# Kernel optimization log

Measured on AMD Instinct MI355X. Metric: run time of the kernel, lower is better.

## Reference

```python
import jax, jax.numpy as jnp
import numpy as np

THRESHOLD = 0.5
NEG_POS_RATIO = 3


def cxcycz_to_xyz(c):
    return jnp.concatenate([c[..., :3] - c[..., 3:] / 2, c[..., :3] + c[..., 3:] / 2], axis=-1)


def xyz_to_cxcycz(x):
    return jnp.concatenate([(x[..., :3] + x[..., 3:]) / 2, x[..., 3:] - x[..., :3]], axis=-1)


def cxcycz_to_gcxgcygcz(c, priors):
    # SSD offset encoding (variance 0.1 / 0.2), 3D version
    return jnp.concatenate([
        (c[..., :3] - priors[..., :3]) / (priors[..., 3:] / 10.0),
        jnp.log(c[..., 3:] / priors[..., 3:]) * 5.0,
    ], axis=-1)


def jaccard3d(a, b):
    # a: [n,6] xyz boxes, b: [m,6] xyz boxes -> [n,m] IoU
    lo = jnp.maximum(a[:, None, :3], b[None, :, :3])
    hi = jnp.minimum(a[:, None, 3:], b[None, :, 3:])
    inter = jnp.prod(jnp.clip(hi - lo, 0.0, None), axis=-1)
    va = jnp.prod(a[:, 3:] - a[:, :3], axis=-1)
    vb = jnp.prod(b[:, 3:] - b[:, :3], axis=-1)
    return inter / (va[:, None] + vb[None, :] - inter)


def setup_inputs() -> dict:
    key = jax.random.key(0)
    ks = jax.random.split(key, 6)
    B, P, n_obj, n_classes = 16, 131072, 16, 2
    predicted_locs = jax.random.normal(ks[0], (B, P, 6), jnp.float32)
    predicted_scores = jax.random.normal(ks[1], (B, P, n_classes), jnp.float32)
    ctr = jax.random.uniform(ks[2], (B, n_obj, 3), minval=0.2, maxval=0.8)
    sz = jax.random.uniform(ks[3], (B, n_obj, 3), minval=0.05, maxval=0.2)
    boxes = jnp.concatenate([ctr - sz / 2, ctr + sz / 2], axis=-1)
    labels = jnp.ones((B, n_obj), jnp.int32)  # single foreground class (lesion)
    pctr = jax.random.uniform(ks[4], (P, 3), minval=0.0, maxval=1.0)
    psz = jax.random.uniform(ks[5], (P, 3), minval=0.05, maxval=0.3)
    priors_cxcycz = jnp.concatenate([pctr, psz], axis=-1)
    return {
        'predicted_locs': predicted_locs,
        'predicted_scores': predicted_scores,
        'boxes': boxes,
        'labels': labels,
        'priors_cxcycz': priors_cxcycz,
    }


def reference(predicted_locs, predicted_scores, boxes, labels, priors_cxcycz):
    B, P, n_classes = predicted_scores.shape
    n_obj = boxes.shape[1]
    priors_xyz = cxcycz_to_xyz(priors_cxcycz)

    def match(boxes_i, labels_i):
        ov = jaccard3d(boxes_i, priors_xyz)              # [n_obj, P]
        overlap_fp = ov.max(axis=0)                      # best overlap per prior
        object_fp = jnp.argmax(ov, axis=0)               # best object per prior
        prior_fo = jnp.argmax(ov, axis=1)                # best prior per object
        # force each object's best prior to be matched to that object
        object_fp = object_fp.at[prior_fo].set(jnp.arange(n_obj))
        overlap_fp = overlap_fp.at[prior_fo].set(1.0)
        lab = jnp.where(overlap_fp < THRESHOLD, 0, labels_i[object_fp])
        tl = cxcycz_to_gcxgcygcz(xyz_to_cxcycz(boxes_i[object_fp]), priors_cxcycz)
        return lab, tl

    true_classes, true_locs = jax.vmap(match)(boxes, labels)  # [B,P], [B,P,6]

    pos = true_classes > 0                               # [B,P]
    n_pos = pos.sum(axis=1)                              # [B]
    total_pos = n_pos.sum()

    # L1Loss(mean) over positive rows of [*,6]
    loc_abs = jnp.abs(predicted_locs - true_locs).sum(axis=-1)   # [B,P]
    loc_loss = (loc_abs * pos).sum() / (total_pos * 6).astype(predicted_locs.dtype)

    # per-prior cross-entropy
    logp = jax.nn.log_softmax(predicted_scores, axis=-1)
    conf_all = -jnp.take_along_axis(logp, true_classes[..., None], axis=-1)[..., 0]
    conf_all = jnp.where(true_classes < 0, 0.0, conf_all)  # ignored priors (soft mode only)
    conf_pos_sum = (conf_all * pos).sum()

    # hard-negative mining: zero out positives, sort each row descending, take top 3*n_pos
    conf_neg = jnp.where(pos, 0.0, conf_all)
    conf_neg_sorted = -jnp.sort(-conf_neg, axis=1)
    hard = jnp.arange(P)[None, :] < (NEG_POS_RATIO * n_pos)[:, None]
    conf_loss = (jnp.where(hard, conf_neg_sorted, 0.0).sum() + conf_pos_sum) / total_pos.astype(predicted_scores.dtype)
    return conf_loss, loc_loss
```

## Files before the change

kernel.cpp:

```cpp
#include <hip/hip_runtime.h>
#include <math.h>

#define MITEMS 2
#define LB 32


template <int NOBJ, bool FULL>
__global__ __launch_bounds__(256) void mbl_match(
    const float* __restrict__ boxes, const float* __restrict__ priors,
    unsigned long long* __restrict__ part_fo, unsigned char* __restrict__ best_u8,
    int P, int n_obj) {
  const int b = blockIdx.y;
  const int tid = threadIdx.x;
  __shared__ float4 s_box[NOBJ][2];
  __shared__ unsigned s_iou[8][257];
  __shared__ unsigned s_inv[8][257];
  __shared__ unsigned long long s_red2[8][33];

  for (int i = tid; i < NOBJ; i += 256) {
    float4 v0, v1;
    if (i < n_obj) {
      const float* bx = boxes + ((size_t)b * n_obj + i) * 6;
      const float l0 = bx[0], l1 = bx[1], l2 = bx[2];
      const float h0 = bx[3], h1 = bx[4], h2 = bx[5];
      v0 = make_float4(l0, l1, l2, h0);
      v1 = make_float4(h1, h2, ((h0 - l0) * (h1 - l1)) * (h2 - l2), 0.f);
    } else {
      v0 = make_float4(3e18f, 3e18f, 3e18f, 1e18f);
      v1 = make_float4(1e18f, 1e18f, 0.f, 0.f);
    }
    s_box[i][0] = v0;
    s_box[i][1] = v1;
  }
  __syncthreads();

  float lo0[MITEMS], lo1[MITEMS], lo2[MITEMS], hi0[MITEMS], hi1[MITEMS],
      hi2[MITEMS], vb[MITEMS];
  unsigned invp[MITEMS];
  const int base = blockIdx.x * (256 * MITEMS);
#pragma unroll
  for (int k = 0; k < MITEMS; ++k) {
    const int p = base + k * 256 + tid;
    if (FULL || p < P) {
      const float2 q0 = *(const float2*)(priors + (size_t)p * 6);
      const float2 q1 = *(const float2*)(priors + (size_t)p * 6 + 2);
      const float2 q2 = *(const float2*)(priors + (size_t)p * 6 + 4);
      lo0[k] = q0.x - q1.y * 0.5f; hi0[k] = q0.x + q1.y * 0.5f;
      lo1[k] = q0.y - q2.x * 0.5f; hi1[k] = q0.y + q2.x * 0.5f;
      lo2[k] = q1.x - q2.y * 0.5f; hi2[k] = q1.x + q2.y * 0.5f;
      vb[k] = (q1.y * q2.x) * q2.y;
      invp[k] = 0xFFFFFFFFu - (unsigned)p;
    } else {
      lo0[k] = lo1[k] = lo2[k] = 3e18f;
      hi0[k] = hi1[k] = hi2[k] = 3e18f;
      vb[k] = 0.f;
      invp[k] = 0u;
    }
  }

  float piou[NOBJ];
  unsigned pinv[NOBJ];
#pragma unroll
  for (int o = 0; o < NOBJ; ++o) { piou[o] = -1.0f; pinv[o] = 0u; }
  float bv[MITEMS];
  int bo[MITEMS];
#pragma unroll
  for (int k = 0; k < MITEMS; ++k) { bv[k] = -1.0f; bo[k] = 0; }

#pragma unroll
  for (int o = 0; o < NOBJ; ++o) {
    const float4 c0 = s_box[o][0];
    const float4 c1 = s_box[o][1];
#pragma unroll
    for (int k = 0; k < MITEMS; ++k) {
      const float d0 = fminf(c0.w, hi0[k]) - fmaxf(c0.x, lo0[k]);
      const float d1 = fminf(c1.x, hi1[k]) - fmaxf(c0.y, lo1[k]);
      const float d2 = fminf(c1.y, hi2[k]) - fmaxf(c0.z, lo2[k]);
      const float inter = (fmaxf(d0, 0.f) * fmaxf(d1, 0.f)) * fmaxf(d2, 0.f);
      const float un = (c1.z + vb[k]) - inter;
      const float iou = inter * __builtin_amdgcn_rcpf(un);
      if (iou > bv[k]) { bv[k] = iou; bo[k] = o; }
      if (iou > piou[o]) { piou[o] = iou; pinv[o] = invp[k]; }
    }
  }

#pragma unroll
  for (int k = 0; k < MITEMS; ++k) {
    const int p = base + k * 256 + tid;
    if (FULL || p < P)
      best_u8[(size_t)b * P + p] =
          (unsigned char)((unsigned)bo[k] | (bv[k] >= 0.5f ? 0x80u : 0u));
  }

  for (int pass = 0; pass < NOBJ / 8; ++pass) {
    if (pass > 0) __syncthreads();
#pragma unroll
    for (int o = 0; o < NOBJ; ++o) {
      if ((o >> 3) == pass) {
        s_iou[o & 7][tid] = __float_as_uint(piou[o]);
        s_inv[o & 7][tid] = pinv[o];
      }
    }
    __syncthreads();
    const int obj8 = tid >> 5, seg = tid & 31;
    unsigned long long m = 0ULL;
#pragma unroll
    for (int i = 0; i < 8; ++i) {
      const int idx = seg + 32 * i;
      const unsigned long long x =
          ((unsigned long long)s_iou[obj8][idx] << 32) | s_inv[obj8][idx];
      if (x > m) m = x;
    }
    s_red2[obj8][seg] = m;
    __syncthreads();
    if (tid < 8) {
      unsigned long long m2 = 0ULL;
      for (int i = 0; i < 32; ++i) {
        const unsigned long long x = s_red2[tid][i];
        if (x > m2) m2 = x;
      }
      const int o = pass * 8 + tid;
      if (o < n_obj)
        part_fo[((size_t)b * gridDim.x + blockIdx.x) * NOBJ + o] = m2;
    }
  }
}

__global__ __launch_bounds__(256) void mbl_reduce_fo(
    const unsigned long long* __restrict__ part_fo,
    unsigned char* __restrict__ best_u8,
    unsigned long long* __restrict__ zero_buf, int zero_words,
    int nblk, int n_obj, int nobjT, int P) {
  const int b = blockIdx.x;
  const int tid = threadIdx.x;
  {
    const int total = (int)gridDim.x * 256;
    for (int i = b * 256 + tid; i < zero_words; i += total) zero_buf[i] = 0ULL;
  }
  __shared__ unsigned s_win[64];
  const int j = tid & 15;
  for (int o0 = 0; o0 < n_obj; o0 += 16) {
    const int o = o0 + (tid >> 4);
    unsigned long long v = 0ULL;
    if (o < n_obj) {
      const unsigned long long* src = part_fo + (size_t)b * nblk * nobjT + o;
      for (int i = j; i < nblk; i += 16) {
        const unsigned long long x = src[(size_t)i * nobjT];
        if (x > v) v = x;
      }
    }
#pragma unroll
    for (int off = 1; off < 16; off <<= 1) {
      const unsigned long long w = __shfl_xor(v, off, 64);
      if (w > v) v = w;
    }
    if (j == 0 && o < n_obj)
      s_win[o] = 0xFFFFFFFFu - (unsigned)(v & 0xFFFFFFFFull);
  }
  __syncthreads();
  if (tid == 0) {
    for (int o = 0; o < n_obj; ++o)
      best_u8[(size_t)b * P + s_win[o]] = (unsigned char)(0x80u | (unsigned)o);
  }
}

template <int CC>
__global__ __launch_bounds__(256) void mbl_loss(
    const float* __restrict__ locs, const float* __restrict__ scores,
    const float* __restrict__ boxes, const int* __restrict__ labels,
    const float* __restrict__ priors, const unsigned char* __restrict__ best_u8,
    float* __restrict__ conf_neg, unsigned* __restrict__ hist0,
    int* __restrict__ n_pos, double* __restrict__ pconf, double* __restrict__ ploc,
    int P, int n_obj, int C) {
  const int b = blockIdx.y;
  const int tid = threadIdx.x;
  __shared__ float s_box[64][6];
  __shared__ int s_lab[64];
  __shared__ unsigned s_hist[4096];
  for (int i = tid; i < 4096; i += 256) s_hist[i] = 0u;
  for (int i = tid; i < n_obj * 6; i += 256)
    s_box[i / 6][i % 6] = boxes[(size_t)b * n_obj * 6 + i];
  for (int i = tid; i < n_obj; i += 256) s_lab[i] = labels[(size_t)b * n_obj + i];
  __syncthreads();

  const int chunk = (P + gridDim.x - 1) / gridDim.x;
  const int start = blockIdx.x * chunk;
  const int end = min(start + chunk, P);
  int np_l = 0;
  double cf_l = 0.0, lc_l = 0.0;
  for (int p = start + tid; p < end; p += 256) {
    const unsigned char bp = best_u8[(size_t)b * P + p];
    const int obj = bp & 0x7F;
    const int posf = bp >> 7;
    const int lab = posf ? s_lab[obj] : 0;

    float conf;
    if (CC == 2) {
      const float2 sc = *(const float2*)(scores + ((size_t)b * P + p) * 2);
      const float m = fmaxf(sc.x, sc.y);
      conf = (lab < 0) ? 0.f
                       : (m + __logf(__expf(sc.x - m) + __expf(sc.y - m)) -
                          ((lab == 0) ? sc.x : sc.y));
    } else {
      const float* sp = scores + ((size_t)b * P + p) * C;
      float m = sp[0];
      for (int c = 1; c < C; ++c) m = fmaxf(m, sp[c]);
      float se = 0.f;
      for (int c = 0; c < C; ++c) se += __expf(sp[c] - m);
      conf = (lab < 0) ? 0.f : (m + __logf(se) - sp[lab]);
    }

    float cn = conf;
    if (lab > 0) {
      np_l++;
      cf_l += (double)conf;
      const float* pr = priors + (size_t)p * 6;
      const float* pl = locs + ((size_t)b * P + p) * 6;
      float ls = 0.f;
      for (int i = 0; i < 3; ++i) {
        const float c0 = (s_box[obj][i] + s_box[obj][i + 3]) * 0.5f;
        const float szb = s_box[obj][i + 3] - s_box[obj][i];
        const float g = (c0 - pr[i]) / (pr[i + 3] / 10.0f);
        const float g2 = logf(szb / pr[i + 3]) * 5.0f;
        ls += fabsf(pl[i] - g) + fabsf(pl[i + 3] - g2);
      }
      lc_l += (double)ls;
      cn = 0.f;
    }
    conf_neg[(size_t)b * P + p] = cn;
    atomicAdd(&s_hist[__float_as_uint(cn) >> 20], 1u);
  }

  __shared__ int r_np[256];
  __shared__ double r_c[256];
  __shared__ double r_l[256];
  r_np[tid] = np_l;
  r_c[tid] = cf_l;
  r_l[tid] = lc_l;
  __syncthreads();
  for (int s = 128; s > 0; s >>= 1) {
    if (tid < s) {
      r_np[tid] += r_np[tid + s];
      r_c[tid] += r_c[tid + s];
      r_l[tid] += r_l[tid + s];
    }
    __syncthreads();
  }
  if (tid == 0 && r_np[0] > 0) {
    atomicAdd(&n_pos[b], r_np[0]);
    atomicAdd(&pconf[b], r_c[0]);
    atomicAdd(&ploc[b], r_l[0]);
  }
  for (int i = tid; i < 4096; i += 256)
    if (s_hist[i]) atomicAdd(&hist0[(size_t)b * 4096 + i], s_hist[i]);
}

template <int BINS>
__device__ void block_select(const unsigned* __restrict__ h, int remk,
                             unsigned* s_scan, int* s_out, unsigned* sel,
                             int* remk_o) {
  constexpr int BPT = BINS / 256;
  const int t = threadIdx.x;
  if (t == 0) { s_out[0] = BINS - 1; s_out[1] = 0; }
  unsigned mb[BPT];
  unsigned s = 0;
#pragma unroll
  for (int i = 0; i < BPT; ++i) { mb[i] = h[t * BPT + i]; s += mb[i]; }
  unsigned incl = s;
  s_scan[t] = incl;
  __syncthreads();
  for (int off = 1; off < 256; off <<= 1) {
    const unsigned add = (t >= off) ? s_scan[t - off] : 0u;
    __syncthreads();
    incl += add;
    s_scan[t] = incl;
    __syncthreads();
  }
  const unsigned total = s_scan[255];
  const unsigned R = total - incl;
  if (remk > 0 && R < (unsigned)remk && R + s >= (unsigned)remk) {
    unsigned acc = R;
    int sel_i = t * BPT, rk = 0;
    bool done = false;
#pragma unroll
    for (int i = BPT - 1; i >= 0; --i) {
      if (!done && acc + mb[i] >= (unsigned)remk) {
        sel_i = t * BPT + i;
        rk = remk - (int)acc;
        done = true;
      }
      if (!done) acc += mb[i];
    }
    s_out[0] = sel_i;
    s_out[1] = rk;
  }
  __syncthreads();
  *sel = (unsigned)s_out[0];
  *remk_o = s_out[1];
  __syncthreads();
}

__global__ __launch_bounds__(256) void mbl_hist1(
    const float* __restrict__ conf_neg, const int* __restrict__ n_pos,
    const unsigned* __restrict__ hist0, unsigned* __restrict__ hist1, int P) {
  const int b = blockIdx.y;
  const int tid = threadIdx.x;
  __shared__ unsigned s_scan[256];
  __shared__ int s_out[2];
  __shared__ unsigned s_hist[4096];
  int K = 3 * n_pos[b];
  if (K > P) K = P;
  unsigned sel0;
  int rem0;
  block_select<4096>(hist0 + (size_t)b * 4096, K, s_scan, s_out, &sel0, &rem0);
  for (int i = tid; i < 4096; i += 256) s_hist[i] = 0u;
  __syncthreads();
  const float* row = conf_neg + (size_t)b * P;
  const int n4 = P >> 2;
  const int per = (n4 + (int)gridDim.x - 1) / (int)gridDim.x;
  const int s4 = blockIdx.x * per, e4 = min(s4 + per, n4);
  for (int i = s4 + tid; i < e4; i += 256) {
    const float4 v = ((const float4*)row)[i];
    unsigned u;
    u = __float_as_uint(v.x); if ((u >> 20) == sel0) atomicAdd(&s_hist[(u >> 8) & 4095u], 1u);
    u = __float_as_uint(v.y); if ((u >> 20) == sel0) atomicAdd(&s_hist[(u >> 8) & 4095u], 1u);
    u = __float_as_uint(v.z); if ((u >> 20) == sel0) atomicAdd(&s_hist[(u >> 8) & 4095u], 1u);
    u = __float_as_uint(v.w); if ((u >> 20) == sel0) atomicAdd(&s_hist[(u >> 8) & 4095u], 1u);
  }
  if (blockIdx.x == 0)
    for (int p = (n4 << 2) + tid; p < P; p += 256) {
      const unsigned u = __float_as_uint(row[p]);
      if ((u >> 20) == sel0) atomicAdd(&s_hist[(u >> 8) & 4095u], 1u);
    }
  __syncthreads();
  for (int i = tid; i < 4096; i += 256)
    if (s_hist[i]) atomicAdd(&hist1[(size_t)b * 4096 + i], s_hist[i]);
}

__global__ __launch_bounds__(256) void mbl_sum(
    const float* __restrict__ conf_neg, const int* __restrict__ n_pos,
    const unsigned* __restrict__ hist0, const unsigned* __restrict__ hist1,
    const double* __restrict__ pconf, const double* __restrict__ ploc,
    double* __restrict__ phard, unsigned* __restrict__ counter,
    int P, int B, float* __restrict__ out) {
  const int b = blockIdx.y;
  const int tid = threadIdx.x;
  __shared__ unsigned s_scan[256];
  __shared__ int s_out[2];
  int K = 3 * n_pos[b];
  if (K > P) K = P;
  unsigned sel0, sel1;
  int rem0, rem1;
  block_select<4096>(hist0 + (size_t)b * 4096, K, s_scan, s_out, &sel0, &rem0);
  block_select<4096>(hist1 + (size_t)b * 4096, rem0, s_scan, s_out, &sel1, &rem1);
  const unsigned pref24 = (sel0 << 12) | sel1;
  const unsigned tb = (pref24 << 8) | 0xFFu;
  const float* row = conf_neg + (size_t)b * P;
  const int n4 = P >> 2;
  const int per = (n4 + (int)gridDim.x - 1) / (int)gridDim.x;
  const int s4 = blockIdx.x * per, e4 = min(s4 + per, n4);
  double local = 0.0;
  for (int i = s4 + tid; i < e4; i += 256) {
    const float4 v = ((const float4*)row)[i];
    if (__float_as_uint(v.x) > tb) local += (double)v.x;
    if (__float_as_uint(v.y) > tb) local += (double)v.y;
    if (__float_as_uint(v.z) > tb) local += (double)v.z;
    if (__float_as_uint(v.w) > tb) local += (double)v.w;
  }
  if (blockIdx.x == 0) {
    for (int p = (n4 << 2) + tid; p < P; p += 256) {
      const float v = row[p];
      if (__float_as_uint(v) > tb) local += (double)v;
    }
    if (tid == 0 && rem1 > 0)
      local += (double)rem1 * (double)__uint_as_float((pref24 << 8) | 0x80u);
  }
  __shared__ double red[256];
  red[tid] = local;
  __syncthreads();
  for (int s = 128; s > 0; s >>= 1) {
    if (tid < s) red[tid] += red[tid + s];
    __syncthreads();
  }
  if (tid == 0) {
    if (red[0] != 0.0) atomicAdd(&phard[b], red[0]);
    __threadfence();
    const unsigned done = atomicAdd(counter, 1u);
    if (done == gridDim.x * gridDim.y - 1) {
      double tp = 0.0, cs = 0.0, ls = 0.0, hs = 0.0;
      for (int i = 0; i < B; ++i) {
        tp += (double)n_pos[i];
        cs += pconf[i];
        ls += ploc[i];
        hs += atomicAdd(&phard[i], 0.0);
      }
      out[0] = (float)((hs + cs) / tp);
      out[1] = (float)(ls / (tp * 6.0));
    }
  }
}

extern "C" void kernel_launch(void* const* d_in, const int* in_sizes, int n_in,
                              void* d_out, int out_size, void* d_ws, size_t ws_size,
                              hipStream_t stream) {
  const float* locs = (const float*)d_in[0];
  const float* scores = (const float*)d_in[1];
  const float* boxes = (const float*)d_in[2];
  const int* labels = (const int*)d_in[3];
  const float* priors = (const float*)d_in[4];

  const long long sz_locs = (long long)in_sizes[0];
  const long long sz_scores = (long long)in_sizes[1];
  const long long sz_priors = (long long)in_sizes[4];
  const int P = (int)(sz_priors / 6);
  const int B = (int)(sz_locs / sz_priors);
  const int n_obj = in_sizes[3] / B;
  const int C = (int)(sz_scores * 6 / sz_locs);

  const int tile = 256 * MITEMS;
  const int nblk = (P + tile - 1) / tile;
  const int nobjT = (n_obj <= 16) ? 16 : ((n_obj <= 32) ? 32 : 64);

  char* ws = (char*)d_ws;
  size_t off = 0;
  double* pconf = (double*)(ws + off); off += (size_t)B * 8;
  double* ploc = (double*)(ws + off); off += (size_t)B * 8;
  double* phard = (double*)(ws + off); off += (size_t)B * 8;
  int* n_pos = (int*)(ws + off); off += ((size_t)B * 4 + 15) & ~(size_t)15;
  unsigned* counter = (unsigned*)(ws + off); off += 16;
  unsigned* hist0 = (unsigned*)(ws + off); off += (size_t)B * 4096 * 4;
  unsigned* hist1 = (unsigned*)(ws + off); off += (size_t)B * 4096 * 4;
  const size_t zero_bytes = off;
  float* conf_neg = (float*)(ws + off); off += ((size_t)B * P * 4 + 15) & ~(size_t)15;
  unsigned char* best_u8 = (unsigned char*)(ws + off);
  off += ((size_t)B * P + 15) & ~(size_t)15;
  unsigned long long* part_fo = (unsigned long long*)(ws + off);
  off += (size_t)B * nblk * nobjT * 8;
  (void)ws_size;

  const dim3 mgrid(nblk, B);
  const bool full = (P % tile) == 0;
  if (n_obj <= 16) {
    if (full) mbl_match<16, true><<<mgrid, 256, 0, stream>>>(boxes, priors, part_fo, best_u8, P, n_obj);
    else      mbl_match<16, false><<<mgrid, 256, 0, stream>>>(boxes, priors, part_fo, best_u8, P, n_obj);
  } else if (n_obj <= 32) {
    if (full) mbl_match<32, true><<<mgrid, 256, 0, stream>>>(boxes, priors, part_fo, best_u8, P, n_obj);
    else      mbl_match<32, false><<<mgrid, 256, 0, stream>>>(boxes, priors, part_fo, best_u8, P, n_obj);
  } else {
    if (full) mbl_match<64, true><<<mgrid, 256, 0, stream>>>(boxes, priors, part_fo, best_u8, P, n_obj);
    else      mbl_match<64, false><<<mgrid, 256, 0, stream>>>(boxes, priors, part_fo, best_u8, P, n_obj);
  }

  mbl_reduce_fo<<<B, 256, 0, stream>>>(part_fo, best_u8, (unsigned long long*)d_ws,
                                       (int)(zero_bytes / 8), nblk, n_obj, nobjT, P);

  const dim3 lgrid(LB, B);
  if (C == 2)
    mbl_loss<2><<<lgrid, 256, 0, stream>>>(locs, scores, boxes, labels, priors,
                                           best_u8, conf_neg, hist0, n_pos, pconf, ploc,
                                           P, n_obj, C);
  else
    mbl_loss<0><<<lgrid, 256, 0, stream>>>(locs, scores, boxes, labels, priors,
                                           best_u8, conf_neg, hist0, n_pos, pconf, ploc,
                                           P, n_obj, C);

  mbl_hist1<<<lgrid, 256, 0, stream>>>(conf_neg, n_pos, hist0, hist1, P);
  mbl_sum<<<lgrid, 256, 0, stream>>>(conf_neg, n_pos, hist0, hist1, pconf, ploc,
                                     phard, counter, P, B, (float*)d_out);
}
```

Baseline: 88.60 us.

## Track max IoU only in match, recover argmax prior in a second pass

The match kernel now keeps only a 32-bit max IoU per object instead of a packed 64-bit (iou, index) pair, and reduces it with shuffles and a global atomicMax. A new recover kernel recomputes IoU only in blocks whose partial max equals the global max, using bit-exact rounding intrinsics, and atomically selects the lowest winning prior index. The loss kernel then applies the forced-positive override by comparing each prior against the per-object winner list, replacing the serial scatter in the old reduce kernel. This lightens register pressure and inner-loop work in match, at the cost of an extra kernel launch, a memset, and a per-prior 16-way compare in the loss kernel.

```diff
diff --git a/kernel.cpp b/kernel.cpp
--- a/kernel.cpp
+++ b/kernel.cpp
@@ -2,66 +2,86 @@
 #include <math.h>
 
 #define MITEMS 2
+#define TILE 512
 #define LB 32
 
+
+__device__ __forceinline__ void prep_prior(const float* __restrict__ pr,
+                                           float& lo0, float& lo1, float& lo2,
+                                           float& hi0, float& hi1, float& hi2,
+                                           float& vb) {
+  const float2 q0 = *(const float2*)(pr);
+  const float2 q1 = *(const float2*)(pr + 2);
+  const float2 q2 = *(const float2*)(pr + 4);
+  const float h0 = __fmul_rn(q1.y, 0.5f);
+  const float h1 = __fmul_rn(q2.x, 0.5f);
+  const float h2 = __fmul_rn(q2.y, 0.5f);
+  lo0 = __fadd_rn(q0.x, -h0); hi0 = __fadd_rn(q0.x, h0);
+  lo1 = __fadd_rn(q0.y, -h1); hi1 = __fadd_rn(q0.y, h1);
+  lo2 = __fadd_rn(q1.x, -h2); hi2 = __fadd_rn(q1.x, h2);
+  vb = __fmul_rn(__fmul_rn(q1.y, q2.x), q2.y);
+}
+
+__device__ __forceinline__ void make_box(const float* __restrict__ bx,
+                                         float4& c0, float4& c1) {
+  const float l0 = bx[0], l1 = bx[1], l2 = bx[2];
+  const float h0 = bx[3], h1 = bx[4], h2 = bx[5];
+  c0 = make_float4(l0, l1, l2, h0);
+  const float vol = __fmul_rn(
+      __fmul_rn(__fadd_rn(h0, -l0), __fadd_rn(h1, -l1)), __fadd_rn(h2, -l2));
+  c1 = make_float4(h1, h2, vol, 0.f);
+}
+
+__device__ __forceinline__ float iou6(float lo0, float lo1, float lo2, float hi0,
+                                      float hi1, float hi2, float vb,
+                                      const float4& c0, const float4& c1) {
+  const float d0 = __fadd_rn(fminf(c0.w, hi0), -fmaxf(c0.x, lo0));
+  const float d1 = __fadd_rn(fminf(c1.x, hi1), -fmaxf(c0.y, lo1));
+  const float d2 = __fadd_rn(fminf(c1.y, hi2), -fmaxf(c0.z, lo2));
+  const float e0 = fmaxf(d0, 0.f), e1 = fmaxf(d1, 0.f), e2 = fmaxf(d2, 0.f);
+  const float inter = __fmul_rn(__fmul_rn(e0, e1), e2);
+  const float un = __fadd_rn(__fadd_rn(c1.z, vb), -inter);
+  return __fmul_rn(inter, __builtin_amdgcn_rcpf(un));
+}
 
 template <int NOBJ, bool FULL>
 __global__ __launch_bounds__(256) void mbl_match(
     const float* __restrict__ boxes, const float* __restrict__ priors,
-    unsigned long long* __restrict__ part_fo, unsigned char* __restrict__ best_u8,
-    int P, int n_obj) {
+    unsigned* __restrict__ part_max, unsigned* __restrict__ M,
+    unsigned char* __restrict__ best_u8, int P, int n_obj) {
   const int b = blockIdx.y;
   const int tid = threadIdx.x;
   __shared__ float4 s_box[NOBJ][2];
-  __shared__ unsigned s_iou[8][257];
-  __shared__ unsigned s_inv[8][257];
-  __shared__ unsigned long long s_red2[8][33];
-
+  __shared__ unsigned s_tr[16][264];
   for (int i = tid; i < NOBJ; i += 256) {
-    float4 v0, v1;
     if (i < n_obj) {
-      const float* bx = boxes + ((size_t)b * n_obj + i) * 6;
-      const float l0 = bx[0], l1 = bx[1], l2 = bx[2];
-      const float h0 = bx[3], h1 = bx[4], h2 = bx[5];
-      v0 = make_float4(l0, l1, l2, h0);
-      v1 = make_float4(h1, h2, ((h0 - l0) * (h1 - l1)) * (h2 - l2), 0.f);
+      make_box(boxes + ((size_t)b * n_obj + i) * 6, s_box[i][0], s_box[i][1]);
     } else {
-      v0 = make_float4(3e18f, 3e18f, 3e18f, 1e18f);
-      v1 = make_float4(1e18f, 1e18f, 0.f, 0.f);
-    }
-    s_box[i][0] = v0;
-    s_box[i][1] = v1;
+      s_box[i][0] = make_float4(3e18f, 3e18f, 3e18f, 1e18f);
+      s_box[i][1] = make_float4(1e18f, 1e18f, 1.0f, 0.f);
+    }
   }
   __syncthreads();
 
   float lo0[MITEMS], lo1[MITEMS], lo2[MITEMS], hi0[MITEMS], hi1[MITEMS],
       hi2[MITEMS], vb[MITEMS];
-  unsigned invp[MITEMS];
-  const int base = blockIdx.x * (256 * MITEMS);
+  const int base = blockIdx.x * TILE;
 #pragma unroll
   for (int k = 0; k < MITEMS; ++k) {
     const int p = base + k * 256 + tid;
     if (FULL || p < P) {
-      const float2 q0 = *(const float2*)(priors + (size_t)p * 6);
-      const float2 q1 = *(const float2*)(priors + (size_t)p * 6 + 2);
-      const float2 q2 = *(const float2*)(priors + (size_t)p * 6 + 4);
-      lo0[k] = q0.x - q1.y * 0.5f; hi0[k] = q0.x + q1.y * 0.5f;
-      lo1[k] = q0.y - q2.x * 0.5f; hi1[k] = q0.y + q2.x * 0.5f;
-      lo2[k] = q1.x - q2.y * 0.5f; hi2[k] = q1.x + q2.y * 0.5f;
-      vb[k] = (q1.y * q2.x) * q2.y;
-      invp[k] = 0xFFFFFFFFu - (unsigned)p;
+      prep_prior(priors + (size_t)p * 6, lo0[k], lo1[k], lo2[k], hi0[k], hi1[k],
+                 hi2[k], vb[k]);
     } else {
       lo0[k] = lo1[k] = lo2[k] = 3e18f;
       hi0[k] = hi1[k] = hi2[k] = 3e18f;
       vb[k] = 0.f;
-      invp[k] = 0u;
     }
   }
 
   float piou[NOBJ];
-  unsigned pinv[NOBJ];
-#pragma unroll
-  for (int o = 0; o < NOBJ; ++o) { piou[o] = -1.0f; pinv[o] = 0u; }
+#pragma unroll
+  for (int o = 0; o < NOBJ; ++o) piou[o] = 0.f;
   float bv[MITEMS];
   int bo[MITEMS];
 #pragma unroll
@@ -73,14 +93,12 @@
     const float4 c1 = s_box[o][1];
 #pragma unroll
     for (int k = 0; k < MITEMS; ++k) {
-      const float d0 = fminf(c0.w, hi0[k]) - fmaxf(c0.x, lo0[k]);
-      const float d1 = fminf(c1.x, hi1[k]) - fmaxf(c0.y, lo1[k]);
-      const float d2 = fminf(c1.y, hi2[k]) - fmaxf(c0.z, lo2[k]);
-      const float inter = (fmaxf(d0, 0.f) * fmaxf(d1, 0.f)) * fmaxf(d2, 0.f);
-      const float un = (c1.z + vb[k]) - inter;
-      const float iou = inter * __builtin_amdgcn_rcpf(un);
-      if (iou > bv[k]) { bv[k] = iou; bo[k] = o; }
-      if (iou > piou[o]) { piou[o] = iou; pinv[o] = invp[k]; }
+      const float iou = iou6(lo0[k], lo1[k], lo2[k], hi0[k], hi1[k], hi2[k],
+                             vb[k], c0, c1);
+      const bool g = iou > bv[k];
+      bv[k] = g ? iou : bv[k];
+      bo[k] = g ? o : bo[k];
+      piou[o] = fmaxf(piou[o], iou);
     }
   }
 
@@ -92,75 +110,74 @@
           (unsigned char)((unsigned)bo[k] | (bv[k] >= 0.5f ? 0x80u : 0u));
   }
 
-  for (int pass = 0; pass < NOBJ / 8; ++pass) {
-    if (pass > 0) __syncthreads();
-#pragma unroll
-    for (int o = 0; o < NOBJ; ++o) {
-      if ((o >> 3) == pass) {
-        s_iou[o & 7][tid] = __float_as_uint(piou[o]);
-        s_inv[o & 7][tid] = pinv[o];
+  for (int o0 = 0; o0 < NOBJ; o0 += 16) {
+    if (o0) __syncthreads();
+#pragma unroll
+    for (int o = 0; o < NOBJ; ++o)
+      if (o >= o0 && o < o0 + 16) s_tr[o - o0][tid] = __float_as_uint(piou[o]);
+    __syncthreads();
+    const int obj = tid >> 4, j = tid & 15;
+    unsigned m = 0u;
+#pragma unroll
+    for (int i = 0; i < 16; ++i) m = max(m, s_tr[obj][j + 16 * i]);
+#pragma unroll
+    for (int off = 1; off < 16; off <<= 1) m = max(m, __shfl_xor(m, off, 64));
+    if (j == 0) {
+      const int o = o0 + obj;
+      if (o < n_obj) {
+        part_max[((size_t)b * gridDim.x + blockIdx.x) * NOBJ + o] = m;
+        atomicMax(&M[(size_t)b * 64 + o], m);
       }
     }
-    __syncthreads();
-    const int obj8 = tid >> 5, seg = tid & 31;
-    unsigned long long m = 0ULL;
-#pragma unroll
-    for (int i = 0; i < 8; ++i) {
-      const int idx = seg + 32 * i;
-      const unsigned long long x =
-          ((unsigned long long)s_iou[obj8][idx] << 32) | s_inv[obj8][idx];
-      if (x > m) m = x;
-    }
-    s_red2[obj8][seg] = m;
-    __syncthreads();
-    if (tid < 8) {
-      unsigned long long m2 = 0ULL;
-      for (int i = 0; i < 32; ++i) {
-        const unsigned long long x = s_red2[tid][i];
-        if (x > m2) m2 = x;
-      }
-      const int o = pass * 8 + tid;
-      if (o < n_obj)
-        part_fo[((size_t)b * gridDim.x + blockIdx.x) * NOBJ + o] = m2;
-    }
-  }
-}
-
-__global__ __launch_bounds__(256) void mbl_reduce_fo(
-    const unsigned long long* __restrict__ part_fo,
-    unsigned char* __restrict__ best_u8,
-    unsigned long long* __restrict__ zero_buf, int zero_words,
-    int nblk, int n_obj, int nobjT, int P) {
-  const int b = blockIdx.x;
+  }
+}
+
+template <bool FULL>
+__global__ __launch_bounds__(256) void mbl_recover(
+    const float* __restrict__ boxes, const float* __restrict__ priors,
+    const unsigned* __restrict__ part_max, const unsigned* __restrict__ M,
+    unsigned* __restrict__ win, unsigned long long* __restrict__ zero_buf,
+    int zero_words, int P, int n_obj, int nobjT) {
+  const int b = blockIdx.y;
+  const int blk = blockIdx.x;
   const int tid = threadIdx.x;
   {
-    const int total = (int)gridDim.x * 256;
-    for (int i = b * 256 + tid; i < zero_words; i += total) zero_buf[i] = 0ULL;
-  }
-  __shared__ unsigned s_win[64];
-  const int j = tid & 15;
-  for (int o0 = 0; o0 < n_obj; o0 += 16) {
-    const int o = o0 + (tid >> 4);
-    unsigned long long v = 0ULL;
-    if (o < n_obj) {
-      const unsigned long long* src = part_fo + (size_t)b * nblk * nobjT + o;
-      for (int i = j; i < nblk; i += 16) {
-        const unsigned long long x = src[(size_t)i * nobjT];
-        if (x > v) v = x;
+    const int gid = b * gridDim.x + blk;
+    const int total = (int)(gridDim.x * gridDim.y) * 256;
+    for (int i = gid * 256 + tid; i < zero_words; i += total) zero_buf[i] = 0ULL;
+  }
+  __shared__ unsigned s_mu[64];
+  __shared__ int s_hit[64];
+  if (tid < 64) {
+    unsigned mu = 0u;
+    int hit = 0;
+    if (tid < n_obj && tid < nobjT) {
+      mu = M[(size_t)b * 64 + tid];
+      const unsigned pm = part_max[((size_t)b * gridDim.x + blk) * nobjT + tid];
+      hit = (pm == mu);
+    }
+    s_mu[tid] = mu;
+    s_hit[tid] = hit;
+  }
+  __syncthreads();
+
+  const int base = blk * TILE;
+  for (int o = 0; o < n_obj; ++o) {
+    if (!s_hit[o]) continue;
+    float4 c0, c1;
+    make_box(boxes + ((size_t)b * n_obj + o) * 6, c0, c1);
+    const unsigned target = s_mu[o];
+#pragma unroll
+    for (int k = 0; k < MITEMS; ++k) {
+      const int p = base + k * 256 + tid;
+      if (FULL || p < P) {
+        float lo0, lo1, lo2, hi0, hi1, hi2, vb;
+        prep_prior(priors + (size_t)p * 6, lo0, lo1, lo2, hi0, hi1, hi2, vb);
+        const float iou = iou6(lo0, lo1, lo2, hi0, hi1, hi2, vb, c0, c1);
+        if (__float_as_uint(iou) == target)
+          atomicMax(&win[(size_t)b * 64 + o], 0xFFFFFFFFu - (unsigned)p);
       }
     }
-#pragma unroll
-    for (int off = 1; off < 16; off <<= 1) {
-      const unsigned long long w = __shfl_xor(v, off, 64);
-      if (w > v) v = w;
-    }
-    if (j == 0 && o < n_obj)
-      s_win[o] = 0xFFFFFFFFu - (unsigned)(v & 0xFFFFFFFFull);
-  }
-  __syncthreads();
-  if (tid == 0) {
-    for (int o = 0; o < n_obj; ++o)
-      best_u8[(size_t)b * P + s_win[o]] = (unsigned char)(0x80u | (unsigned)o);
   }
 }
 
@@ -168,20 +185,32 @@
 __global__ __launch_bounds__(256) void mbl_loss(
     const float* __restrict__ locs, const float* __restrict__ scores,
     const float* __restrict__ boxes, const int* __restrict__ labels,
-    const float* __restrict__ priors, const unsigned char* __restrict__ best_u8,
-    float* __restrict__ conf_neg, unsigned* __restrict__ hist0,
-    int* __restrict__ n_pos, double* __restrict__ pconf, double* __restrict__ ploc,
-    int P, int n_obj, int C) {
+    const float* __restrict__ priors, const unsigned* __restrict__ win,
+    const unsigned char* __restrict__ best_u8, float* __restrict__ conf_neg,
+    unsigned* __restrict__ hist0, int* __restrict__ n_pos,
+    double* __restrict__ pconf, double* __restrict__ ploc, int P, int n_obj,
+    int C) {
   const int b = blockIdx.y;
   const int tid = threadIdx.x;
   __shared__ float s_box[64][6];
   __shared__ int s_lab[64];
+  __shared__ unsigned s_fo[64];
   __shared__ unsigned s_hist[4096];
   for (int i = tid; i < 4096; i += 256) s_hist[i] = 0u;
   for (int i = tid; i < n_obj * 6; i += 256)
     s_box[i / 6][i % 6] = boxes[(size_t)b * n_obj * 6 + i];
-  for (int i = tid; i < n_obj; i += 256) s_lab[i] = labels[(size_t)b * n_obj + i];
-  __syncthreads();
+  for (int i = tid; i < n_obj; i += 256) {
+    s_lab[i] = labels[(size_t)b * n_obj + i];
+    s_fo[i] = 0xFFFFFFFFu - win[(size_t)b * 64 + i];
+  }
+  __syncthreads();
+
+  unsigned fo_r[16];
+  const bool small_obj = (n_obj <= 16);
+  if (small_obj) {
+#pragma unroll
+    for (int o = 0; o < 16; ++o) fo_r[o] = (o < n_obj) ? s_fo[o] : 0xFFFFFFFEu;
+  }
 
   const int chunk = (P + gridDim.x - 1) / gridDim.x;
   const int start = blockIdx.x * chunk;
@@ -190,8 +219,16 @@
   double cf_l = 0.0, lc_l = 0.0;
   for (int p = start + tid; p < end; p += 256) {
     const unsigned char bp = best_u8[(size_t)b * P + p];
-    const int obj = bp & 0x7F;
-    const int posf = bp >> 7;
+    int obj = bp & 0x7F;
+    int posf = bp >> 7;
+    if (small_obj) {
+#pragma unroll
+      for (int o = 0; o < 16; ++o)
+        if (fo_r[o] == (unsigned)p) { obj = o; posf = 1; }
+    } else {
+      for (int o = 0; o < n_obj; ++o)
+        if (s_fo[o] == (unsigned)p) { obj = o; posf = 1; }
+    }
     const int lab = posf ? s_lab[obj] : 0;
 
     float conf;
@@ -341,8 +378,8 @@
     const float* __restrict__ conf_neg, const int* __restrict__ n_pos,
     const unsigned* __restrict__ hist0, const unsigned* __restrict__ hist1,
     const double* __restrict__ pconf, const double* __restrict__ ploc,
-    double* __restrict__ phard, unsigned* __restrict__ counter,
-    int P, int B, float* __restrict__ out) {
+    double* __restrict__ phard, unsigned* __restrict__ counter, int P, int B,
+    float* __restrict__ out) {
   const int b = blockIdx.y;
   const int tid = threadIdx.x;
   __shared__ unsigned s_scan[256];
@@ -417,8 +454,7 @@
   const int n_obj = in_sizes[3] / B;
   const int C = (int)(sz_scores * 6 / sz_locs);
 
-  const int tile = 256 * MITEMS;
-  const int nblk = (P + tile - 1) / tile;
+  const int nblk = (P + TILE - 1) / TILE;
   const int nobjT = (n_obj <= 16) ? 16 : ((n_obj <= 32) ? 32 : 64);
 
   char* ws = (char*)d_ws;
@@ -428,41 +464,52 @@
   double* phard = (double*)(ws + off); off += (size_t)B * 8;
   int* n_pos = (int*)(ws + off); off += ((size_t)B * 4 + 15) & ~(size_t)15;
   unsigned* counter = (unsigned*)(ws + off); off += 16;
+  unsigned* M = (unsigned*)(ws + off); off += (size_t)B * 64 * 4;
+  unsigned* win = (unsigned*)(ws + off); off += (size_t)B * 64 * 4;
+  const size_t header_bytes = off;
   unsigned* hist0 = (unsigned*)(ws + off); off += (size_t)B * 4096 * 4;
   unsigned* hist1 = (unsigned*)(ws + off); off += (size_t)B * 4096 * 4;
-  const size_t zero_bytes = off;
+  const size_t hist_bytes = (size_t)B * 4096 * 4 * 2;
   float* conf_neg = (float*)(ws + off); off += ((size_t)B * P * 4 + 15) & ~(size_t)15;
   unsigned char* best_u8 = (unsigned char*)(ws + off);
   off += ((size_t)B * P + 15) & ~(size_t)15;
-  unsigned long long* part_fo = (unsigned long long*)(ws + off);
-  off += (size_t)B * nblk * nobjT * 8;
+  unsigned* part_max = (unsigned*)(ws + off);
+  off += (size_t)B * nblk * nobjT * 4;
   (void)ws_size;
 
+  hipMemsetAsync(d_ws, 0, header_bytes, stream);
+
   const dim3 mgrid(nblk, B);
-  const bool full = (P % tile) == 0;
+  const bool full = (P % TILE) == 0;
   if (n_obj <= 16) {
-    if (full) mbl_match<16, true><<<mgrid, 256, 0, stream>>>(boxes, priors, part_fo, best_u8, P, n_obj);
-    else      mbl_match<16, false><<<mgrid, 256, 0, stream>>>(boxes, priors, part_fo, best_u8, P, n_obj);
+    if (full) mbl_match<16, true><<<mgrid, 256, 0, stream>>>(boxes, priors, part_max, M, best_u8, P, n_obj);
+    else      mbl_match<16, false><<<mgrid, 256, 0, stream>>>(boxes, priors, part_max, M, best_u8, P, n_obj);
   } else if (n_obj <= 32) {
-    if (full) mbl_match<32, true><<<mgrid, 256, 0, stream>>>(boxes, priors, part_fo, best_u8, P, n_obj);
-    else      mbl_match<32, false><<<mgrid, 256, 0, stream>>>(boxes, priors, part_fo, best_u8, P, n_obj);
+    if (full) mbl_match<32, true><<<mgrid, 256, 0, stream>>>(boxes, priors, part_max, M, best_u8, P, n_obj);
+    else      mbl_match<32, false><<<mgrid, 256, 0, stream>>>(boxes, priors, part_max, M, best_u8, P, n_obj);
   } else {
-    if (full) mbl_match<64, true><<<mgrid, 256, 0, stream>>>(boxes, priors, part_fo, best_u8, P, n_obj);
-    else      mbl_match<64, false><<<mgrid, 256, 0, stream>>>(boxes, priors, part_fo, best_u8, P, n_obj);
-  }
-
-  mbl_reduce_fo<<<B, 256, 0, stream>>>(part_fo, best_u8, (unsigned long long*)d_ws,
-                                       (int)(zero_bytes / 8), nblk, n_obj, nobjT, P);
+    if (full) mbl_match<64, true><<<mgrid, 256, 0, stream>>>(boxes, priors, part_max, M, best_u8, P, n_obj);
+    else      mbl_match<64, false><<<mgrid, 256, 0, stream>>>(boxes, priors, part_max, M, best_u8, P, n_obj);
+  }
+
+  if (full)
+    mbl_recover<true><<<mgrid, 256, 0, stream>>>(boxes, priors, part_max, M, win,
+                                                 (unsigned long long*)hist0,
+                                                 (int)(hist_bytes / 8), P, n_obj, nobjT);
+  else
+    mbl_recover<false><<<mgrid, 256, 0, stream>>>(boxes, priors, part_max, M, win,
+                                                  (unsigned long long*)hist0,
+                                                  (int)(hist_bytes / 8), P, n_obj, nobjT);
 
   const dim3 lgrid(LB, B);
   if (C == 2)
-    mbl_loss<2><<<lgrid, 256, 0, stream>>>(locs, scores, boxes, labels, priors,
-                                           best_u8, conf_neg, hist0, n_pos, pconf, ploc,
-                                           P, n_obj, C);
+    mbl_loss<2><<<lgrid, 256, 0, stream>>>(locs, scores, boxes, labels, priors, win,
+                                           best_u8, conf_neg, hist0, n_pos, pconf,
+                                           ploc, P, n_obj, C);
   else
-    mbl_loss<0><<<lgrid, 256, 0, stream>>>(locs, scores, boxes, labels, priors,
-                                           best_u8, conf_neg, hist0, n_pos, pconf, ploc,
-                                           P, n_obj, C);
+    mbl_loss<0><<<lgrid, 256, 0, stream>>>(locs, scores, boxes, labels, priors, win,
+                                           best_u8, conf_neg, hist0, n_pos, pconf,
+                                           ploc, P, n_obj, C);
 
   mbl_hist1<<<lgrid, 256, 0, stream>>>(conf_neg, n_pos, hist0, hist1, P);
   mbl_sum<<<lgrid, 256, 0, stream>>>(conf_neg, n_pos, hist0, hist1, pconf, ploc,
```

Result: slower. 103.0 us (+16.3%).

## Fuse per-object best-prior reduction via atomicMax and apply forced matches in loss

Applied to the files above, without the earlier changes.

Removes the separate reduce kernel by having each match block reduce per-object best priors through a shared-memory transpose and global 64-bit atomicMax into a small per-batch buffer. The forced object-to-prior override now happens inside the loss kernel by comparing each prior index against the winning indices. The match kernel drops to one prior per thread with a packed IoU/object-index max. The C==2 loss path processes two priors per thread with vector loads, and workspace zeroing moves to hipMemsetAsync. This trades a kernel launch and partial buffer traffic for global atomics and extra per-prior compares in the loss pass.

```diff
diff --git a/kernel.cpp b/kernel.cpp
--- a/kernel.cpp
+++ b/kernel.cpp
@@ -1,22 +1,23 @@
 #include <hip/hip_runtime.h>
 #include <math.h>
 
-#define MITEMS 2
 #define LB 32
 
 
+__device__ __forceinline__ unsigned long long umax64(unsigned long long a,
+                                                     unsigned long long b) {
+  return a > b ? a : b;
+}
+
 template <int NOBJ, bool FULL>
-__global__ __launch_bounds__(256) void mbl_match(
+__global__ __launch_bounds__(256, 8) void mbl_match(
     const float* __restrict__ boxes, const float* __restrict__ priors,
-    unsigned long long* __restrict__ part_fo, unsigned char* __restrict__ best_u8,
+    unsigned long long* __restrict__ prior_fo, unsigned char* __restrict__ best_u8,
     int P, int n_obj) {
   const int b = blockIdx.y;
   const int tid = threadIdx.x;
   __shared__ float4 s_box[NOBJ][2];
-  __shared__ unsigned s_iou[8][257];
-  __shared__ unsigned s_inv[8][257];
-  __shared__ unsigned long long s_red2[8][33];
-
+  __shared__ unsigned s_tr[16][264];
   for (int i = tid; i < NOBJ; i += 256) {
     float4 v0, v1;
     if (i < n_obj) {
@@ -34,133 +35,68 @@
   }
   __syncthreads();
 
-  float lo0[MITEMS], lo1[MITEMS], lo2[MITEMS], hi0[MITEMS], hi1[MITEMS],
-      hi2[MITEMS], vb[MITEMS];
-  unsigned invp[MITEMS];
-  const int base = blockIdx.x * (256 * MITEMS);
-#pragma unroll
-  for (int k = 0; k < MITEMS; ++k) {
-    const int p = base + k * 256 + tid;
-    if (FULL || p < P) {
-      const float2 q0 = *(const float2*)(priors + (size_t)p * 6);
-      const float2 q1 = *(const float2*)(priors + (size_t)p * 6 + 2);
-      const float2 q2 = *(const float2*)(priors + (size_t)p * 6 + 4);
-      lo0[k] = q0.x - q1.y * 0.5f; hi0[k] = q0.x + q1.y * 0.5f;
-      lo1[k] = q0.y - q2.x * 0.5f; hi1[k] = q0.y + q2.x * 0.5f;
-      lo2[k] = q1.x - q2.y * 0.5f; hi2[k] = q1.x + q2.y * 0.5f;
-      vb[k] = (q1.y * q2.x) * q2.y;
-      invp[k] = 0xFFFFFFFFu - (unsigned)p;
-    } else {
-      lo0[k] = lo1[k] = lo2[k] = 3e18f;
-      hi0[k] = hi1[k] = hi2[k] = 3e18f;
-      vb[k] = 0.f;
-      invp[k] = 0u;
-    }
-  }
-
-  float piou[NOBJ];
-  unsigned pinv[NOBJ];
-#pragma unroll
-  for (int o = 0; o < NOBJ; ++o) { piou[o] = -1.0f; pinv[o] = 0u; }
-  float bv[MITEMS];
-  int bo[MITEMS];
-#pragma unroll
-  for (int k = 0; k < MITEMS; ++k) { bv[k] = -1.0f; bo[k] = 0; }
-
-#pragma unroll
-  for (int o = 0; o < NOBJ; ++o) {
-    const float4 c0 = s_box[o][0];
-    const float4 c1 = s_box[o][1];
-#pragma unroll
-    for (int k = 0; k < MITEMS; ++k) {
-      const float d0 = fminf(c0.w, hi0[k]) - fmaxf(c0.x, lo0[k]);
-      const float d1 = fminf(c1.x, hi1[k]) - fmaxf(c0.y, lo1[k]);
-      const float d2 = fminf(c1.y, hi2[k]) - fmaxf(c0.z, lo2[k]);
+  const int pbase = blockIdx.x * 256;
+  const int p = pbase + tid;
+  float lo0, lo1, lo2, hi0, hi1, hi2, vb;
+  if (FULL || p < P) {
+    const float2 q0 = *(const float2*)(priors + (size_t)p * 6);
+    const float2 q1 = *(const float2*)(priors + (size_t)p * 6 + 2);
+    const float2 q2 = *(const float2*)(priors + (size_t)p * 6 + 4);
+    lo0 = q0.x - q1.y * 0.5f; hi0 = q0.x + q1.y * 0.5f;
+    lo1 = q0.y - q2.x * 0.5f; hi1 = q0.y + q2.x * 0.5f;
+    lo2 = q1.x - q2.y * 0.5f; hi2 = q1.x + q2.y * 0.5f;
+    vb = (q1.y * q2.x) * q2.y;
+  } else {
+    lo0 = lo1 = lo2 = 3e18f;
+    hi0 = hi1 = hi2 = 3e18f;
+    vb = 0.f;
+  }
+
+  const unsigned msk = ~(unsigned)(NOBJ - 1);
+  unsigned pk = 0u;
+
+  for (int o0 = 0; o0 < NOBJ; o0 += 16) {
+    if (o0) __syncthreads();
+#pragma unroll
+    for (int oo = 0; oo < 16; ++oo) {
+      const int o = o0 + oo;
+      const float4 c0 = s_box[o][0];
+      const float4 c1 = s_box[o][1];
+      const float d0 = fminf(c0.w, hi0) - fmaxf(c0.x, lo0);
+      const float d1 = fminf(c1.x, hi1) - fmaxf(c0.y, lo1);
+      const float d2 = fminf(c1.y, hi2) - fmaxf(c0.z, lo2);
       const float inter = (fmaxf(d0, 0.f) * fmaxf(d1, 0.f)) * fmaxf(d2, 0.f);
-      const float un = (c1.z + vb[k]) - inter;
+      const float un = (c1.z + vb) - inter;
       const float iou = inter * __builtin_amdgcn_rcpf(un);
-      if (iou > bv[k]) { bv[k] = iou; bo[k] = o; }
-      if (iou > piou[o]) { piou[o] = iou; pinv[o] = invp[k]; }
-    }
-  }
-
-#pragma unroll
-  for (int k = 0; k < MITEMS; ++k) {
-    const int p = base + k * 256 + tid;
-    if (FULL || p < P)
-      best_u8[(size_t)b * P + p] =
-          (unsigned char)((unsigned)bo[k] | (bv[k] >= 0.5f ? 0x80u : 0u));
-  }
-
-  for (int pass = 0; pass < NOBJ / 8; ++pass) {
-    if (pass > 0) __syncthreads();
-#pragma unroll
-    for (int o = 0; o < NOBJ; ++o) {
-      if ((o >> 3) == pass) {
-        s_iou[o & 7][tid] = __float_as_uint(piou[o]);
-        s_inv[o & 7][tid] = pinv[o];
-      }
+      s_tr[oo][tid] = __float_as_uint(iou);
+      const unsigned cand =
+          (__float_as_uint(iou) & msk) | (unsigned)(NOBJ - 1 - o);
+      pk = max(pk, cand);
     }
     __syncthreads();
-    const int obj8 = tid >> 5, seg = tid & 31;
+    const int obj = tid >> 4, j = tid & 15;
     unsigned long long m = 0ULL;
 #pragma unroll
-    for (int i = 0; i < 8; ++i) {
-      const int idx = seg + 32 * i;
+    for (int i = 0; i < 16; ++i) {
+      const int col = j + 16 * i;
       const unsigned long long x =
-          ((unsigned long long)s_iou[obj8][idx] << 32) | s_inv[obj8][idx];
-      if (x > m) m = x;
-    }
-    s_red2[obj8][seg] = m;
-    __syncthreads();
-    if (tid < 8) {
-      unsigned long long m2 = 0ULL;
-      for (int i = 0; i < 32; ++i) {
-        const unsigned long long x = s_red2[tid][i];
-        if (x > m2) m2 = x;
-      }
-      const int o = pass * 8 + tid;
-      if (o < n_obj)
-        part_fo[((size_t)b * gridDim.x + blockIdx.x) * NOBJ + o] = m2;
-    }
-  }
-}
-
-__global__ __launch_bounds__(256) void mbl_reduce_fo(
-    const unsigned long long* __restrict__ part_fo,
-    unsigned char* __restrict__ best_u8,
-    unsigned long long* __restrict__ zero_buf, int zero_words,
-    int nblk, int n_obj, int nobjT, int P) {
-  const int b = blockIdx.x;
-  const int tid = threadIdx.x;
-  {
-    const int total = (int)gridDim.x * 256;
-    for (int i = b * 256 + tid; i < zero_words; i += total) zero_buf[i] = 0ULL;
-  }
-  __shared__ unsigned s_win[64];
-  const int j = tid & 15;
-  for (int o0 = 0; o0 < n_obj; o0 += 16) {
-    const int o = o0 + (tid >> 4);
-    unsigned long long v = 0ULL;
-    if (o < n_obj) {
-      const unsigned long long* src = part_fo + (size_t)b * nblk * nobjT + o;
-      for (int i = j; i < nblk; i += 16) {
-        const unsigned long long x = src[(size_t)i * nobjT];
-        if (x > v) v = x;
-      }
-    }
-#pragma unroll
-    for (int off = 1; off < 16; off <<= 1) {
-      const unsigned long long w = __shfl_xor(v, off, 64);
-      if (w > v) v = w;
-    }
-    if (j == 0 && o < n_obj)
-      s_win[o] = 0xFFFFFFFFu - (unsigned)(v & 0xFFFFFFFFull);
-  }
-  __syncthreads();
-  if (tid == 0) {
-    for (int o = 0; o < n_obj; ++o)
-      best_u8[(size_t)b * P + s_win[o]] = (unsigned char)(0x80u | (unsigned)o);
+          ((unsigned long long)s_tr[obj][col] << 32) |
+          (0xFFFFFFFFu - (unsigned)(pbase + col));
+      m = umax64(m, x);
+    }
+#pragma unroll
+    for (int off = 1; off < 16; off <<= 1)
+      m = umax64(m, __shfl_xor(m, off, 64));
+    if (j == 0) {
+      const int o = o0 + obj;
+      if (o < n_obj) atomicMax(&prior_fo[(size_t)b * 64 + o], m);
+    }
+  }
+
+  if (FULL || p < P) {
+    const int bo = (NOBJ - 1) - (int)(pk & (unsigned)(NOBJ - 1));
+    best_u8[(size_t)b * P + p] =
+        (unsigned char)((unsigned)bo | (pk >= 0x3F000000u ? 0x80u : 0u));
   }
 }
 
@@ -168,67 +104,127 @@
 __global__ __launch_bounds__(256) void mbl_loss(
     const float* __restrict__ locs, const float* __restrict__ scores,
     const float* __restrict__ boxes, const int* __restrict__ labels,
-    const float* __restrict__ priors, const unsigned char* __restrict__ best_u8,
-    float* __restrict__ conf_neg, unsigned* __restrict__ hist0,
-    int* __restrict__ n_pos, double* __restrict__ pconf, double* __restrict__ ploc,
-    int P, int n_obj, int C) {
+    const float* __restrict__ priors, const unsigned long long* __restrict__ prior_fo,
+    const unsigned char* __restrict__ best_u8, float* __restrict__ conf_neg,
+    unsigned* __restrict__ hist0, int* __restrict__ n_pos,
+    double* __restrict__ pconf, double* __restrict__ ploc, int P, int n_obj,
+    int C) {
   const int b = blockIdx.y;
   const int tid = threadIdx.x;
   __shared__ float s_box[64][6];
   __shared__ int s_lab[64];
+  __shared__ unsigned s_fo[64];
   __shared__ unsigned s_hist[4096];
   for (int i = tid; i < 4096; i += 256) s_hist[i] = 0u;
   for (int i = tid; i < n_obj * 6; i += 256)
     s_box[i / 6][i % 6] = boxes[(size_t)b * n_obj * 6 + i];
-  for (int i = tid; i < n_obj; i += 256) s_lab[i] = labels[(size_t)b * n_obj + i];
-  __syncthreads();
-
-  const int chunk = (P + gridDim.x - 1) / gridDim.x;
-  const int start = blockIdx.x * chunk;
-  const int end = min(start + chunk, P);
+  for (int i = tid; i < n_obj; i += 256) {
+    s_lab[i] = labels[(size_t)b * n_obj + i];
+    s_fo[i] = 0xFFFFFFFFu - (unsigned)(prior_fo[(size_t)b * 64 + i] & 0xFFFFFFFFull);
+  }
+  __syncthreads();
+
+  unsigned fo_r[16];
+  const bool small_obj = (n_obj <= 16);
+  if (small_obj) {
+#pragma unroll
+    for (int o = 0; o < 16; ++o) fo_r[o] = (o < n_obj) ? s_fo[o] : 0xFFFFFFFEu;
+  }
+
   int np_l = 0;
   double cf_l = 0.0, lc_l = 0.0;
-  for (int p = start + tid; p < end; p += 256) {
-    const unsigned char bp = best_u8[(size_t)b * P + p];
-    const int obj = bp & 0x7F;
-    const int posf = bp >> 7;
-    const int lab = posf ? s_lab[obj] : 0;
-
-    float conf;
-    if (CC == 2) {
-      const float2 sc = *(const float2*)(scores + ((size_t)b * P + p) * 2);
-      const float m = fmaxf(sc.x, sc.y);
-      conf = (lab < 0) ? 0.f
-                       : (m + __logf(__expf(sc.x - m) + __expf(sc.y - m)) -
-                          ((lab == 0) ? sc.x : sc.y));
-    } else {
+
+  if (CC == 2 && (P & 1) == 0) {
+    const int P2 = P >> 1;
+    const int chunk = (P2 + (int)gridDim.x - 1) / (int)gridDim.x;
+    const int start = blockIdx.x * chunk;
+    const int end = min(start + chunk, P2);
+    for (int q = start + tid; q < end; q += 256) {
+      const float4 sc = *(const float4*)(scores + ((size_t)b * P2 + q) * 4);
+      const unsigned short bpp =
+          *(const unsigned short*)(best_u8 + (size_t)b * P + 2 * q);
+      float cn2[2];
+#pragma unroll
+      for (int e = 0; e < 2; ++e) {
+        const int p = 2 * q + e;
+        const unsigned bp = e ? (bpp >> 8) : (bpp & 0xFFu);
+        int obj = bp & 0x7F;
+        int posf = (int)(bp >> 7);
+        if (small_obj) {
+#pragma unroll
+          for (int o = 0; o < 16; ++o)
+            if (fo_r[o] == (unsigned)p) { obj = o; posf = 1; }
+        } else {
+          for (int o = 0; o < n_obj; ++o)
+            if (s_fo[o] == (unsigned)p) { obj = o; posf = 1; }
+        }
+        const int lab = posf ? s_lab[obj] : 0;
+        const float sx = e ? sc.z : sc.x;
+        const float sy = e ? sc.w : sc.y;
+        const float mm = fmaxf(sx, sy);
+        const float conf =
+            (lab < 0) ? 0.f
+                      : (mm + __logf(__expf(sx - mm) + __expf(sy - mm)) -
+                         ((lab == 0) ? sx : sy));
+        float cn = conf;
+        if (lab > 0) {
+          np_l++;
+          cf_l += (double)conf;
+          const float* pr = priors + (size_t)p * 6;
+          const float* pl = locs + ((size_t)b * P + p) * 6;
+          float ls = 0.f;
+          for (int i = 0; i < 3; ++i) {
+            const float c0 = (s_box[obj][i] + s_box[obj][i + 3]) * 0.5f;
+            const float szb = s_box[obj][i + 3] - s_box[obj][i];
+            const float g = (c0 - pr[i]) / (pr[i + 3] / 10.0f);
+            const float g2 = logf(szb / pr[i + 3]) * 5.0f;
+            ls += fabsf(pl[i] - g) + fabsf(pl[i + 3] - g2);
+          }
+          lc_l += (double)ls;
+          cn = 0.f;
+        }
+        cn2[e] = cn;
+        atomicAdd(&s_hist[__float_as_uint(cn) >> 20], 1u);
+      }
+      *(float2*)(conf_neg + (size_t)b * P + 2 * q) = make_float2(cn2[0], cn2[1]);
+    }
+  } else {
+    const int chunk = (P + (int)gridDim.x - 1) / (int)gridDim.x;
+    const int start = blockIdx.x * chunk;
+    const int end = min(start + chunk, P);
+    for (int p = start + tid; p < end; p += 256) {
+      const unsigned char bp = best_u8[(size_t)b * P + p];
+      int obj = bp & 0x7F;
+      int posf = bp >> 7;
+      for (int o = 0; o < n_obj; ++o)
+        if (s_fo[o] == (unsigned)p) { obj = o; posf = 1; }
+      const int lab = posf ? s_lab[obj] : 0;
       const float* sp = scores + ((size_t)b * P + p) * C;
       float m = sp[0];
       for (int c = 1; c < C; ++c) m = fmaxf(m, sp[c]);
       float se = 0.f;
       for (int c = 0; c < C; ++c) se += __expf(sp[c] - m);
-      conf = (lab < 0) ? 0.f : (m + __logf(se) - sp[lab]);
-    }
-
-    float cn = conf;
-    if (lab > 0) {
-      np_l++;
-      cf_l += (double)conf;
-      const float* pr = priors + (size_t)p * 6;
-      const float* pl = locs + ((size_t)b * P + p) * 6;
-      float ls = 0.f;
-      for (int i = 0; i < 3; ++i) {
-        const float c0 = (s_box[obj][i] + s_box[obj][i + 3]) * 0.5f;
-        const float szb = s_box[obj][i + 3] - s_box[obj][i];
-        const float g = (c0 - pr[i]) / (pr[i + 3] / 10.0f);
-        const float g2 = logf(szb / pr[i + 3]) * 5.0f;
-        ls += fabsf(pl[i] - g) + fabsf(pl[i + 3] - g2);
+      const float conf = (lab < 0) ? 0.f : (m + __logf(se) - sp[lab]);
+      float cn = conf;
+      if (lab > 0) {
+        np_l++;
+        cf_l += (double)conf;
+        const float* pr = priors + (size_t)p * 6;
+        const float* pl = locs + ((size_t)b * P + p) * 6;
+        float ls = 0.f;
+        for (int i = 0; i < 3; ++i) {
+          const float c0 = (s_box[obj][i] + s_box[obj][i + 3]) * 0.5f;
+          const float szb = s_box[obj][i + 3] - s_box[obj][i];
+          const float g = (c0 - pr[i]) / (pr[i + 3] / 10.0f);
+          const float g2 = logf(szb / pr[i + 3]) * 5.0f;
+          ls += fabsf(pl[i] - g) + fabsf(pl[i + 3] - g2);
+        }
+        lc_l += (double)ls;
+        cn = 0.f;
       }
-      lc_l += (double)ls;
-      cn = 0.f;
-    }
-    conf_neg[(size_t)b * P + p] = cn;
-    atomicAdd(&s_hist[__float_as_uint(cn) >> 20], 1u);
+      conf_neg[(size_t)b * P + p] = cn;
+      atomicAdd(&s_hist[__float_as_uint(cn) >> 20], 1u);
+    }
   }
 
   __shared__ int r_np[256];
@@ -341,8 +337,8 @@
     const float* __restrict__ conf_neg, const int* __restrict__ n_pos,
     const unsigned* __restrict__ hist0, const unsigned* __restrict__ hist1,
     const double* __restrict__ pconf, const double* __restrict__ ploc,
-    double* __restrict__ phard, unsigned* __restrict__ counter,
-    int P, int B, float* __restrict__ out) {
+    double* __restrict__ phard, unsigned* __restrict__ counter, int P, int B,
+    float* __restrict__ out) {
   const int b = blockIdx.y;
   const int tid = threadIdx.x;
   __shared__ unsigned s_scan[256];
@@ -417,10 +413,6 @@
   const int n_obj = in_sizes[3] / B;
   const int C = (int)(sz_scores * 6 / sz_locs);
 
-  const int tile = 256 * MITEMS;
-  const int nblk = (P + tile - 1) / tile;
-  const int nobjT = (n_obj <= 16) ? 16 : ((n_obj <= 32) ? 32 : 64);
-
   char* ws = (char*)d_ws;
   size_t off = 0;
   double* pconf = (double*)(ws + off); off += (size_t)B * 8;
@@ -428,41 +420,41 @@
   double* phard = (double*)(ws + off); off += (size_t)B * 8;
   int* n_pos = (int*)(ws + off); off += ((size_t)B * 4 + 15) & ~(size_t)15;
   unsigned* counter = (unsigned*)(ws + off); off += 16;
+  unsigned long long* prior_fo = (unsigned long long*)(ws + off);
+  off += (size_t)B * 64 * 8;
   unsigned* hist0 = (unsigned*)(ws + off); off += (size_t)B * 4096 * 4;
   unsigned* hist1 = (unsigned*)(ws + off); off += (size_t)B * 4096 * 4;
   const size_t zero_bytes = off;
   float* conf_neg = (float*)(ws + off); off += ((size_t)B * P * 4 + 15) & ~(size_t)15;
   unsigned char* best_u8 = (unsigned char*)(ws + off);
   off += ((size_t)B * P + 15) & ~(size_t)15;
-  unsigned long long* part_fo = (unsigned long long*)(ws + off);
-  off += (size_t)B * nblk * nobjT * 8;
   (void)ws_size;
 
+  hipMemsetAsync(d_ws, 0, zero_bytes, stream);
+
+  const int nblk = (P + 255) / 256;
   const dim3 mgrid(nblk, B);
-  const bool full = (P % tile) == 0;
+  const bool full = (P % 256) == 0;
   if (n_obj <= 16) {
-    if (full) mbl_match<16, true><<<mgrid, 256, 0, stream>>>(boxes, priors, part_fo, best_u8, P, n_obj);
-    else      mbl_match<16, false><<<mgrid, 256, 0, stream>>>(boxes, priors, part_fo, best_u8, P, n_obj);
+    if (full) mbl_match<16, true><<<mgrid, 256, 0, stream>>>(boxes, priors, prior_fo, best_u8, P, n_obj);
+    else      mbl_match<16, false><<<mgrid, 256, 0, stream>>>(boxes, priors, prior_fo, best_u8, P, n_obj);
   } else if (n_obj <= 32) {
-    if (full) mbl_match<32, true><<<mgrid, 256, 0, stream>>>(boxes, priors, part_fo, best_u8, P, n_obj);
-    else      mbl_match<32, false><<<mgrid, 256, 0, stream>>>(boxes, priors, part_fo, best_u8, P, n_obj);
+    if (full) mbl_match<32, true><<<mgrid, 256, 0, stream>>>(boxes, priors, prior_fo, best_u8, P, n_obj);
+    else      mbl_match<32, false><<<mgrid, 256, 0, stream>>>(boxes, priors, prior_fo, best_u8, P, n_obj);
   } else {
-    if (full) mbl_match<64, true><<<mgrid, 256, 0, stream>>>(boxes, priors, part_fo, best_u8, P, n_obj);
-    else      mbl_match<64, false><<<mgrid, 256, 0, stream>>>(boxes, priors, part_fo, best_u8, P, n_obj);
-  }
-
-  mbl_reduce_fo<<<B, 256, 0, stream>>>(part_fo, best_u8, (unsigned long long*)d_ws,
-                                       (int)(zero_bytes / 8), nblk, n_obj, nobjT, P);
+    if (full) mbl_match<64, true><<<mgrid, 256, 0, stream>>>(boxes, priors, prior_fo, best_u8, P, n_obj);
+    else      mbl_match<64, false><<<mgrid, 256, 0, stream>>>(boxes, priors, prior_fo, best_u8, P, n_obj);
+  }
 
   const dim3 lgrid(LB, B);
   if (C == 2)
     mbl_loss<2><<<lgrid, 256, 0, stream>>>(locs, scores, boxes, labels, priors,
-                                           best_u8, conf_neg, hist0, n_pos, pconf, ploc,
-                                           P, n_obj, C);
+                                           prior_fo, best_u8, conf_neg, hist0, n_pos,
+                                           pconf, ploc, P, n_obj, C);
   else
     mbl_loss<0><<<lgrid, 256, 0, stream>>>(locs, scores, boxes, labels, priors,
-                                           best_u8, conf_neg, hist0, n_pos, pconf, ploc,
-                                           P, n_obj, C);
+                                           prior_fo, best_u8, conf_neg, hist0, n_pos,
+                                           pconf, ploc, P, n_obj, C);
 
   mbl_hist1<<<lgrid, 256, 0, stream>>>(conf_neg, n_pos, hist0, hist1, P);
   mbl_sum<<<lgrid, 256, 0, stream>>>(conf_neg, n_pos, hist0, hist1, pconf, ploc,
```

Result: slower. 102.9 us (+16.1%).
